# Kernel tuning notes

Measured on AMD Instinct MI355X. Metric: run time of the kernel, lower is better.

The kernel has to match this reference:

```python
import jax, jax.numpy as jnp
import numpy as np
from jax import lax

N_CHANNEL = 3
CONV_K = 3
POOL_K = 3
LEAKY_SLOPE = 0.01  # torch nn.LeakyReLU default


def setup_inputs() -> dict:
    key = jax.random.key(0)
    k1, k2, k3 = jax.random.split(key, 3)
    B, T, H, W = 8, 16, 256, 256
    x = jax.random.normal(k1, (B, T * N_CHANNEL, H, W), dtype=jnp.float32)
    # Conv2d(in=2*n_channel, out=1, k=3), torch default init ~ U(-bound, bound)
    fan_in = 2 * N_CHANNEL * CONV_K * CONV_K
    bound = 1.0 / np.sqrt(fan_in)
    conv_w = jax.random.uniform(k2, (1, 2 * N_CHANNEL, CONV_K, CONV_K), jnp.float32, -bound, bound)
    conv_b = jax.random.uniform(k3, (1,), jnp.float32, -bound, bound)
    return {"input_tensor": x, "conv_w": conv_w, "conv_b": conv_b}


def _pools(x):
    pp = POOL_K // 2
    dims = (1, 1, POOL_K, POOL_K)
    strides = (1, 1, 1, 1)
    pad = [(0, 0), (0, 0), (pp, pp), (pp, pp)]
    mx = lax.reduce_window(x, -jnp.inf, lax.max, dims, strides, pad)
    # torch AvgPool2d default count_include_pad=True -> divide by k*k everywhere
    av = lax.reduce_window(x, 0.0, lax.add, dims, strides, pad) / (POOL_K * POOL_K)
    return mx, av


def reference(input_tensor, conv_w, conv_b):
    B, Ctot, H, W = input_tensor.shape
    T = Ctot // N_CHANNEL
    cp = CONV_K // 2

    mx, av = _pools(input_tensor)  # each [B, Ctot, H, W]
    # interleave per-channel: [max_0, avg_0, max_1, avg_1, ...]
    pooled = jnp.stack([mx, av], axis=2).reshape(B, 2 * Ctot, H, W)
    # per-timestep conv on its 2*n_channel block -> fold T into batch
    pooled = pooled.reshape(B * T, 2 * N_CHANNEL, H, W)
    y = lax.conv_general_dilated(
        pooled, conv_w, window_strides=(1, 1), padding=[(cp, cp), (cp, cp)],
        dimension_numbers=("NCHW", "OIHW", "NCHW"))
    y = y + conv_b[None, :, None, None]
    y = jnp.where(y >= 0, y, LEAKY_SLOPE * y)  # LeakyReLU
    # broadcast each timestep's 1-channel mask to its n_channel block
    mask = jnp.broadcast_to(y.reshape(B, T, 1, H, W), (B, T, N_CHANNEL, H, W))
    mask = mask.reshape(B, Ctot, H, W)
    return jax.nn.sigmoid(mask)
```

## Files before the change

### kernel.cpp

```cpp
#include <hip/hip_runtime.h>
#include <math.h>


#define H 256
#define W 256
#define NEG_INF (-__builtin_inff())

__device__ __forceinline__ float uniform_f(float v) {
    return __int_as_float(__builtin_amdgcn_readfirstlane(__float_as_int(v)));
}

__global__ __launch_bounds__(256, 6)
void cbam_fused_kernel(const float* __restrict__ x,
                       const float* __restrict__ cw,
                       const float* __restrict__ cb,
                       float* __restrict__ out)
{
    const int tid  = threadIdx.x;
    const int lane = tid & 63;
    const int wy   = tid >> 6;
    const int row  = blockIdx.x * 4 + wy;
    const int bt   = blockIdx.y;
    const int c0   = lane * 4;

    const bool lane0  = (lane == 0);
    const bool lane63 = (lane == 63);

    const bool pv[3] = { row - 1 >= 0, true, row + 1 < H };

    float acc0 = 0.f, acc1 = 0.f, acc2 = 0.f, acc3 = 0.f;

    #pragma unroll 1
    for (int c = 0; c < 3; ++c) {
        const float* ch = x + (size_t)(bt * 3 + c) * (H * W);

        float wm[9];
        #pragma unroll
        for (int k = 0; k < 9; ++k)
            wm[k] = uniform_f(cw[(2 * c) * 9 + k]);

        float wae[5][3];
        #pragma unroll
        for (int r = -2; r <= 2; ++r) {
            #pragma unroll
            for (int kw = 0; kw < 3; ++kw) {
                float s = 0.f;
                #pragma unroll
                for (int p = -1; p <= 1; ++p) {
                    if (p < r - 1 || p > r + 1) continue;
                    const float wv = cw[(2 * c + 1) * 9 + (p + 1) * 3 + kw] * (1.f / 9.f);
                    s += pv[p + 1] ? wv : 0.f;
                }
                wae[r + 2][kw] = uniform_f(s);
            }
        }

        float pm[3][6];
        #pragma unroll
        for (int q = 0; q < 3; ++q)
            #pragma unroll
            for (int j = 0; j < 6; ++j)
                pm[q][j] = NEG_INF;

        #pragma unroll
        for (int r = -2; r <= 2; ++r) {
            const int gr = row + r;
            if (gr >= 0 && gr < H) {
                const float* rp = ch + (size_t)gr * W;
                const float4 L = *(const float4*)(rp + (lane0  ? 0  : c0 - 4));
                const float4 M = *(const float4*)(rp + c0);
                const float4 R = *(const float4*)(rp + (lane63 ? c0 : c0 + 4));

                const float z2 = lane0  ? 0.f : L.z;
                const float z3 = lane0  ? 0.f : L.w;
                const float z8 = lane63 ? 0.f : R.x;
                const float z9 = lane63 ? 0.f : R.y;
                const float m2 = lane0  ? NEG_INF : L.z;
                const float m3 = lane0  ? NEG_INF : L.w;
                const float m8 = lane63 ? NEG_INF : R.x;
                const float m9 = lane63 ? NEG_INF : R.y;

                float rm[6], rs[6];
                rm[0] = fmaxf(fmaxf(m2,  m3),  M.x);  rs[0] = z2 + z3 + M.x;
                rm[1] = fmaxf(fmaxf(m3,  M.x), M.y);  rs[1] = z3 + M.x + M.y;
                rm[2] = fmaxf(fmaxf(M.x, M.y), M.z);  rs[2] = M.x + M.y + M.z;
                rm[3] = fmaxf(fmaxf(M.y, M.z), M.w);  rs[3] = M.y + M.z + M.w;
                rm[4] = fmaxf(fmaxf(M.z, M.w), m8);   rs[4] = M.z + M.w + z8;
                rm[5] = fmaxf(fmaxf(M.w, m8),  m9);   rs[5] = M.w + z8 + z9;

                rs[0] = lane0  ? 0.f : rs[0];
                rs[5] = lane63 ? 0.f : rs[5];

                const float w0 = wae[r + 2][0], w1 = wae[r + 2][1], w2 = wae[r + 2][2];
                acc0 = fmaf(w0, rs[0], fmaf(w1, rs[1], fmaf(w2, rs[2], acc0)));
                acc1 = fmaf(w0, rs[1], fmaf(w1, rs[2], fmaf(w2, rs[3], acc1)));
                acc2 = fmaf(w0, rs[2], fmaf(w1, rs[3], fmaf(w2, rs[4], acc2)));
                acc3 = fmaf(w0, rs[3], fmaf(w1, rs[4], fmaf(w2, rs[5], acc3)));

                #pragma unroll
                for (int q = 0; q < 3; ++q) {
                    const int p = q - 1;
                    if (p < r - 1 || p > r + 1) continue;
                    #pragma unroll
                    for (int j = 0; j < 6; ++j)
                        pm[q][j] = fmaxf(pm[q][j], rm[j]);
                }
            }

            if (r >= 0) {
                const int q = r;
                if (pv[q]) {
                    const float p0 = lane0  ? 0.f : pm[q][0];
                    const float p5 = lane63 ? 0.f : pm[q][5];
                    const float k0 = wm[q * 3 + 0], k1 = wm[q * 3 + 1], k2 = wm[q * 3 + 2];
                    acc0 = fmaf(k0, p0,       fmaf(k1, pm[q][1], fmaf(k2, pm[q][2], acc0)));
                    acc1 = fmaf(k0, pm[q][1], fmaf(k1, pm[q][2], fmaf(k2, pm[q][3], acc1)));
                    acc2 = fmaf(k0, pm[q][2], fmaf(k1, pm[q][3], fmaf(k2, pm[q][4], acc2)));
                    acc3 = fmaf(k0, pm[q][3], fmaf(k1, pm[q][4], fmaf(k2, p5,       acc3)));
                }
            }
        }
    }

    const float bias = uniform_f(cb[0]);
    float4 res;
    {
        float a[4] = { acc0, acc1, acc2, acc3 };
        float* rp = (float*)&res;
        #pragma unroll
        for (int i = 0; i < 4; ++i) {
            float y = a[i] + bias;
            y = (y >= 0.f) ? y : 0.01f * y;
            rp[i] = 1.f / (1.f + expf(-y));
        }
    }
    float* ob = out + (size_t)(bt * 3) * (H * W) + (size_t)row * W + c0;
    *(float4*)(ob)             = res;
    *(float4*)(ob + H * W)     = res;
    *(float4*)(ob + 2 * H * W) = res;
}

extern "C" void kernel_launch(void* const* d_in, const int* in_sizes, int n_in,
                              void* d_out, int out_size, void* d_ws, size_t ws_size,
                              hipStream_t stream) {
    const float* x  = (const float*)d_in[0];
    const float* cw = (const float*)d_in[1];
    const float* cb = (const float*)d_in[2];
    float* out = (float*)d_out;

    const int BT_in  = in_sizes[0] / (3 * H * W);
    const int BT_out = out_size    / (3 * H * W);
    if (BT_in <= 0 || BT_in != BT_out ||
        in_sizes[0] != BT_in * 3 * H * W || out_size != BT_in * 3 * H * W ||
        n_in < 3 || in_sizes[1] < 54 || in_sizes[2] < 1)
        return;

    dim3 grid(H / 4, BT_in);
    dim3 block(256);
    cbam_fused_kernel<<<grid, block, 0, stream>>>(x, cw, cb, out);
}
```

Measured before the change: 232.0 us.

## Compute four output rows per wavefront with rolling pooled-row buffers

Each wavefront now produces four consecutive output rows instead of one, streaming eight input rows through a rolling three-slot buffer of row-wise max and sum pools. The change is meant to cut redundant global loads and pooling arithmetic, since the five-row halo per output row becomes eight rows per four output rows. The grid shrinks by a factor of four and the launch-bounds occupancy hint drops to four blocks, so register pressure rises and parallelism falls.

```diff
diff --git a/kernel.cpp b/kernel.cpp
--- a/kernel.cpp
+++ b/kernel.cpp
@@ -10,7 +10,7 @@
     return __int_as_float(__builtin_amdgcn_readfirstlane(__float_as_int(v)));
 }
 
-__global__ __launch_bounds__(256, 6)
+__global__ __launch_bounds__(256, 4)
 void cbam_fused_kernel(const float* __restrict__ x,
                        const float* __restrict__ cw,
                        const float* __restrict__ cb,
@@ -18,54 +18,46 @@
 {
     const int tid  = threadIdx.x;
     const int lane = tid & 63;
-    const int wy   = tid >> 6;
-    const int row  = blockIdx.x * 4 + wy;
+    const int wq   = tid >> 6;
+    const int rb   = blockIdx.x * 16 + wq * 4;
     const int bt   = blockIdx.y;
     const int c0   = lane * 4;
 
     const bool lane0  = (lane == 0);
     const bool lane63 = (lane == 63);
+    const bool top = (rb == 0);
+    const bool bot = (rb == H - 4);
 
-    const bool pv[3] = { row - 1 >= 0, true, row + 1 < H };
-
-    float acc0 = 0.f, acc1 = 0.f, acc2 = 0.f, acc3 = 0.f;
+    float acc[4][4];
+    #pragma unroll
+    for (int o = 0; o < 4; ++o)
+        #pragma unroll
+        for (int j = 0; j < 4; ++j) acc[o][j] = 0.f;
 
     #pragma unroll 1
     for (int c = 0; c < 3; ++c) {
         const float* ch = x + (size_t)(bt * 3 + c) * (H * W);
 
-        float wm[9];
+        float wm[9], wa[9];
         #pragma unroll
-        for (int k = 0; k < 9; ++k)
+        for (int k = 0; k < 9; ++k) {
             wm[k] = uniform_f(cw[(2 * c) * 9 + k]);
-
-        float wae[5][3];
-        #pragma unroll
-        for (int r = -2; r <= 2; ++r) {
-            #pragma unroll
-            for (int kw = 0; kw < 3; ++kw) {
-                float s = 0.f;
-                #pragma unroll
-                for (int p = -1; p <= 1; ++p) {
-                    if (p < r - 1 || p > r + 1) continue;
-                    const float wv = cw[(2 * c + 1) * 9 + (p + 1) * 3 + kw] * (1.f / 9.f);
-                    s += pv[p + 1] ? wv : 0.f;
-                }
-                wae[r + 2][kw] = uniform_f(s);
-            }
+            wa[k] = uniform_f(cw[(2 * c + 1) * 9 + k] * (1.f / 9.f));
         }
 
-        float pm[3][6];
-        #pragma unroll
-        for (int q = 0; q < 3; ++q)
-            #pragma unroll
-            for (int j = 0; j < 6; ++j)
-                pm[q][j] = NEG_INF;
+        float pm[3][6], ps[3][6];
 
         #pragma unroll
-        for (int r = -2; r <= 2; ++r) {
-            const int gr = row + r;
-            if (gr >= 0 && gr < H) {
+        for (int i = 0; i < 8; ++i) {
+            if (i <= 5) {
+                const int q = i % 3;
+                #pragma unroll
+                for (int j = 0; j < 6; ++j) { pm[q][j] = NEG_INF; ps[q][j] = 0.f; }
+            }
+
+            const int gr = rb - 2 + i;
+            const bool rowvalid = (i >= 2 && i <= 5) ? true : (i < 2 ? !top : !bot);
+            if (rowvalid) {
                 const float* rp = ch + (size_t)gr * W;
                 const float4 L = *(const float4*)(rp + (lane0  ? 0  : c0 - 4));
                 const float4 M = *(const float4*)(rp + c0);
@@ -87,57 +79,69 @@
                 rm[3] = fmaxf(fmaxf(M.y, M.z), M.w);  rs[3] = M.y + M.z + M.w;
                 rm[4] = fmaxf(fmaxf(M.z, M.w), m8);   rs[4] = M.z + M.w + z8;
                 rm[5] = fmaxf(fmaxf(M.w, m8),  m9);   rs[5] = M.w + z8 + z9;
-
                 rs[0] = lane0  ? 0.f : rs[0];
                 rs[5] = lane63 ? 0.f : rs[5];
 
-                const float w0 = wae[r + 2][0], w1 = wae[r + 2][1], w2 = wae[r + 2][2];
-                acc0 = fmaf(w0, rs[0], fmaf(w1, rs[1], fmaf(w2, rs[2], acc0)));
-                acc1 = fmaf(w0, rs[1], fmaf(w1, rs[2], fmaf(w2, rs[3], acc1)));
-                acc2 = fmaf(w0, rs[2], fmaf(w1, rs[3], fmaf(w2, rs[4], acc2)));
-                acc3 = fmaf(w0, rs[3], fmaf(w1, rs[4], fmaf(w2, rs[5], acc3)));
-
                 #pragma unroll
-                for (int q = 0; q < 3; ++q) {
-                    const int p = q - 1;
-                    if (p < r - 1 || p > r + 1) continue;
+                for (int d = -2; d <= 0; ++d) {
+                    const int pr = i + d;
+                    if (pr < 0 || pr > 5) continue;
+                    const int q = pr % 3;
                     #pragma unroll
-                    for (int j = 0; j < 6; ++j)
+                    for (int j = 0; j < 6; ++j) {
                         pm[q][j] = fmaxf(pm[q][j], rm[j]);
+                        ps[q][j] += rs[j];
+                    }
                 }
             }
 
-            if (r >= 0) {
-                const int q = r;
-                if (pv[q]) {
-                    const float p0 = lane0  ? 0.f : pm[q][0];
-                    const float p5 = lane63 ? 0.f : pm[q][5];
-                    const float k0 = wm[q * 3 + 0], k1 = wm[q * 3 + 1], k2 = wm[q * 3 + 2];
-                    acc0 = fmaf(k0, p0,       fmaf(k1, pm[q][1], fmaf(k2, pm[q][2], acc0)));
-                    acc1 = fmaf(k0, pm[q][1], fmaf(k1, pm[q][2], fmaf(k2, pm[q][3], acc1)));
-                    acc2 = fmaf(k0, pm[q][2], fmaf(k1, pm[q][3], fmaf(k2, pm[q][4], acc2)));
-                    acc3 = fmaf(k0, pm[q][3], fmaf(k1, pm[q][4], fmaf(k2, p5,       acc3)));
+            if (i >= 2) {
+                const int pr = i - 2;
+                const int q = pr % 3;
+                const bool pvalid = (pr >= 1 && pr <= 4) ? true
+                                                         : (pr == 0 ? !top : !bot);
+                if (pvalid) {
+                    const float P0 = lane0  ? 0.f : pm[q][0];
+                    const float P5 = lane63 ? 0.f : pm[q][5];
+                    const float P1 = pm[q][1], P2 = pm[q][2],
+                                P3 = pm[q][3], P4 = pm[q][4];
+                    #pragma unroll
+                    for (int orel = pr - 2; orel <= pr; ++orel) {
+                        if (orel < 0 || orel > 3) continue;
+                        const int kr = pr - orel;
+                        const float km0 = wm[kr*3+0], km1 = wm[kr*3+1], km2 = wm[kr*3+2];
+                        const float ka0 = wa[kr*3+0], ka1 = wa[kr*3+1], ka2 = wa[kr*3+2];
+                        acc[orel][0] = fmaf(km0,P0, fmaf(km1,P1, fmaf(km2,P2, acc[orel][0])));
+                        acc[orel][1] = fmaf(km0,P1, fmaf(km1,P2, fmaf(km2,P3, acc[orel][1])));
+                        acc[orel][2] = fmaf(km0,P2, fmaf(km1,P3, fmaf(km2,P4, acc[orel][2])));
+                        acc[orel][3] = fmaf(km0,P3, fmaf(km1,P4, fmaf(km2,P5, acc[orel][3])));
+                        acc[orel][0] = fmaf(ka0,ps[q][0], fmaf(ka1,ps[q][1], fmaf(ka2,ps[q][2], acc[orel][0])));
+                        acc[orel][1] = fmaf(ka0,ps[q][1], fmaf(ka1,ps[q][2], fmaf(ka2,ps[q][3], acc[orel][1])));
+                        acc[orel][2] = fmaf(ka0,ps[q][2], fmaf(ka1,ps[q][3], fmaf(ka2,ps[q][4], acc[orel][2])));
+                        acc[orel][3] = fmaf(ka0,ps[q][3], fmaf(ka1,ps[q][4], fmaf(ka2,ps[q][5], acc[orel][3])));
+                    }
                 }
             }
         }
     }
 
     const float bias = uniform_f(cb[0]);
-    float4 res;
-    {
-        float a[4] = { acc0, acc1, acc2, acc3 };
+    float* ob = out + (size_t)(bt * 3) * (H * W) + (size_t)rb * W + c0;
+    #pragma unroll
+    for (int o = 0; o < 4; ++o) {
+        float4 res;
         float* rp = (float*)&res;
         #pragma unroll
-        for (int i = 0; i < 4; ++i) {
-            float y = a[i] + bias;
+        for (int j = 0; j < 4; ++j) {
+            float y = acc[o][j] + bias;
             y = (y >= 0.f) ? y : 0.01f * y;
-            rp[i] = 1.f / (1.f + expf(-y));
+            rp[j] = 1.f / (1.f + expf(-y));
         }
+        float* obr = ob + (size_t)o * W;
+        *(float4*)(obr)              = res;
+        *(float4*)(obr + H * W)      = res;
+        *(float4*)(obr + 2 * H * W)  = res;
     }
-    float* ob = out + (size_t)(bt * 3) * (H * W) + (size_t)row * W + c0;
-    *(float4*)(ob)             = res;
-    *(float4*)(ob + H * W)     = res;
-    *(float4*)(ob + 2 * H * W) = res;
 }
 
 extern "C" void kernel_launch(void* const* d_in, const int* in_sizes, int n_in,
@@ -155,7 +159,7 @@
         n_in < 3 || in_sizes[1] < 54 || in_sizes[2] < 1)
         return;
 
-    dim3 grid(H / 4, BT_in);
+    dim3 grid(H / 16, BT_in);
     dim3 block(256);
     cbam_fused_kernel<<<grid, block, 0, stream>>>(x, cw, cb, out);
 }
```

Result: slower. 382.7 us (+65.0%).
